# Performance work log

Hardware: AMD Instinct MI355X
Metric: run time of the kernel (lower is better)

## Reference

```python
import jax, jax.numpy as jnp
import numpy as np

B, M, D = 4, 2048, 1024


def setup_inputs() -> dict:
    key = jax.random.key(0)
    k1, k2, k3, k4 = jax.random.split(key, 4)
    x = jax.random.normal(k1, (B, M, D), dtype=jnp.float32)
    scale = 0.02
    wq = jax.random.normal(k2, (D, D), dtype=jnp.float32) * scale
    wk = jax.random.normal(k3, (D, D), dtype=jnp.float32) * scale
    wv = jax.random.normal(k4, (D, D), dtype=jnp.float32) * scale
    return {"x": x, "wq": wq, "wk": wk, "wv": wv}


def _rope_tables(m, d):
    # Faithful to source: phi = 10000 ** (-2*(i-1)/d)  (note the (i-1), incl. i=0)
    i = jnp.arange(d // 2, dtype=jnp.float32)
    phi = jnp.power(10000.0, -2.0 * (i - 1.0) / d)  # [d/2]
    pos = jnp.arange(m, dtype=jnp.float32)
    ang = pos[:, None] * phi[None, :]  # [m, d/2]
    return jnp.cos(ang), jnp.sin(ang)


def _apply_rope(t, cos, sin):
    # Original does t[pos] @ R[pos] (row-vector times rotation matrix):
    #   out_even =  t_even*cos + t_odd*sin
    #   out_odd  = -t_even*sin + t_odd*cos
    te = t[..., 0::2]  # [b, m, d/2]
    to = t[..., 1::2]
    oe = te * cos + to * sin
    oo = -te * sin + to * cos
    return jnp.stack([oe, oo], axis=-1).reshape(t.shape)


def reference(x, wq, wk, wv):
    b, m, d = x.shape
    q = x @ wq.T
    k = x @ wk.T
    v = x @ wv.T
    cos, sin = _rope_tables(m, d)
    qr = _apply_rope(q, cos, sin)
    kr = _apply_rope(k, cos, sin)
    # causal SDPA (dropout disabled for deterministic reference)
    scores = jnp.einsum('bqd,bkd->bqk', qr, kr) / jnp.sqrt(jnp.float32(d))
    causal = jnp.tril(jnp.ones((m, m), dtype=bool))
    scores = jnp.where(causal[None, :, :], scores, jnp.finfo(scores.dtype).min)
    attn = jax.nn.softmax(scores, axis=-1)
    return jnp.einsum('bqk,bkd->bqd', attn, v)
```

## Files before the change

kernel.cpp:

```cpp
#include <hip/hip_runtime.h>
#include <hip/hip_bf16.h>
#include <math.h>


typedef __bf16 bf16x8 __attribute__((ext_vector_type(8)));
typedef float  f32x4  __attribute__((ext_vector_type(4)));

__device__ __forceinline__ ushort f2bf(float f) {
    __hip_bfloat16 h = __float2bfloat16(f);
    return *reinterpret_cast<ushort*>(&h);
}

__device__ __forceinline__ void async_load16(const ushort* g, ushort* l) {
    __builtin_amdgcn_global_load_lds(
        (const __attribute__((address_space(1))) void*)g,
        (__attribute__((address_space(3))) void*)l, 16, 0, 0);
}

__global__ __launch_bounds__(256) void cvt_kernel(
    const float* __restrict__ in, ushort* __restrict__ out, int n4)
{
    int i = blockIdx.x * blockDim.x + threadIdx.x;
    if (i < n4) {
        float4 f = ((const float4*)in)[i];
        ushort4 o;
        o.x = f2bf(f.x); o.y = f2bf(f.y); o.z = f2bf(f.z); o.w = f2bf(f.w);
        ((ushort4*)out)[i] = o;
    }
}

__device__ __forceinline__ void gemm128_core(
    const ushort* __restrict__ A, const ushort* __restrict__ B,
    int lda, int ldb, int m0, int n0, int kIters,
    ushort* As, ushort* Bs, f32x4 acc[4][4])
{
    const int tid  = threadIdx.x;
    const int lane = tid & 63, wave = tid >> 6;
    const int wm = (wave >> 1) * 64, wn = (wave & 1) * 64;
    const int quad = lane >> 4, l16 = lane & 15;
    const int srow = lane >> 2, scol = (lane & 3) * 8;

    const ushort* ag0 = A + (size_t)(m0 + wave * 32 + srow) * lda + scol;
    const ushort* bg0 = B + (size_t)(n0 + wave * 32 + srow) * ldb + scol;
    const ushort* ag1 = ag0 + (size_t)16 * lda;
    const ushort* bg1 = bg0 + (size_t)16 * ldb;
    ushort* la0 = As + (wave * 32) * 32;
    ushort* la1 = As + (wave * 32 + 16) * 32;
    ushort* lb0 = Bs + (wave * 32) * 32;
    ushort* lb1 = Bs + (wave * 32 + 16) * 32;

    for (int kt = 0; kt < kIters; ++kt) {
        const int k0 = kt * 32;
        async_load16(ag0 + k0, la0);
        async_load16(ag1 + k0, la1);
        async_load16(bg0 + k0, lb0);
        async_load16(bg1 + k0, lb1);
        __syncthreads();
        bf16x8 aF[4], bF[4];
#pragma unroll
        for (int i = 0; i < 4; ++i)
            aF[i] = *(const bf16x8*)(As + (wm + i * 16 + l16) * 32 + quad * 8);
#pragma unroll
        for (int j = 0; j < 4; ++j)
            bF[j] = *(const bf16x8*)(Bs + (wn + j * 16 + l16) * 32 + quad * 8);
#pragma unroll
        for (int i = 0; i < 4; ++i)
#pragma unroll
            for (int j = 0; j < 4; ++j)
                acc[i][j] = __builtin_amdgcn_mfma_f32_16x16x32_bf16(aF[i], bF[j], acc[i][j], 0, 0, 0);
        __syncthreads();
    }
}

#define ACC_INIT(acc) \
    _Pragma("unroll") for (int i = 0; i < 4; ++i) \
    _Pragma("unroll") for (int j = 0; j < 4; ++j) \
    _Pragma("unroll") for (int r = 0; r < 4; ++r) acc[i][j][r] = 0.0f;

__global__ __launch_bounds__(256) void qkv_rope_kernel(
    const ushort* __restrict__ xb, const ushort* __restrict__ wq,
    const ushort* __restrict__ wk, const ushort* __restrict__ wv,
    ushort* __restrict__ Qr, ushort* __restrict__ Kr, ushort* __restrict__ VT)
{
    __shared__ __attribute__((aligned(16))) ushort As[128 * 32];
    __shared__ __attribute__((aligned(16))) ushort Bs[128 * 32];
    const int m0 = blockIdx.x * 128;
    const int n0 = blockIdx.y * 128;
    const int z  = blockIdx.z;
    const ushort* W = (z == 0) ? wq : (z == 1) ? wk : wv;

    f32x4 acc[4][4];
    ACC_INIT(acc)
    gemm128_core(xb, W, 1024, 1024, m0, n0, 32, As, Bs, acc);

    const int lane = threadIdx.x & 63, wave = threadIdx.x >> 6;
    const int wm = (wave >> 1) * 64, wn = (wave & 1) * 64;
    const int quad = lane >> 4, l16 = lane & 15;

    if (z < 2) {
        ushort* out = (z == 0) ? Qr : Kr;
#pragma unroll
        for (int j = 0; j < 4; ++j) {
            const int n = n0 + wn + j * 16 + l16;
            const float phi = powf(10000.0f, -2.0f * ((float)(n >> 1) - 1.0f) / 1024.0f);
            float sphi, cphi;
            sincosf(phi, &sphi, &cphi);
#pragma unroll
            for (int i = 0; i < 4; ++i) {
                const int mbase = m0 + wm + i * 16 + quad * 4;
                const int pos0  = mbase & 2047;
                float s, c;
                sincosf((float)pos0 * phi, &s, &c);
#pragma unroll
                for (int r = 0; r < 4; ++r) {
                    float v = acc[i][j][r];
                    float p = __shfl_xor(v, 1);
                    float o = (n & 1) ? (v * c - p * s) : (v * c + p * s);
                    out[(size_t)(mbase + r) * 1024 + n] = f2bf(o);
                    float s2 = s * cphi + c * sphi;
                    c = c * cphi - s * sphi;
                    s = s2;
                }
            }
        }
    } else {
#pragma unroll
        for (int i = 0; i < 4; ++i) {
            const int mbase = m0 + wm + i * 16 + quad * 4;
            const int b = mbase >> 11, pos0 = mbase & 2047;
#pragma unroll
            for (int j = 0; j < 4; ++j) {
                const int n = n0 + wn + j * 16 + l16;
                ushort4 o;
                o.x = f2bf(acc[i][j][0]); o.y = f2bf(acc[i][j][1]);
                o.z = f2bf(acc[i][j][2]); o.w = f2bf(acc[i][j][3]);
                *(ushort4*)(VT + ((size_t)b * 1024 + n) * 2048 + pos0) = o;
            }
        }
    }
}

__global__ __launch_bounds__(256) void scores_kernel(
    const ushort* __restrict__ Qr, const ushort* __restrict__ Kr,
    float* __restrict__ S)
{
    const int m0 = blockIdx.x * 128;
    const int n0 = blockIdx.y * 128;
    if (n0 > m0 + 127) return;
    const int b = blockIdx.z;
    __shared__ __attribute__((aligned(16))) ushort As[128 * 32];
    __shared__ __attribute__((aligned(16))) ushort Bs[128 * 32];
    const ushort* A = Qr + (size_t)b * 2048 * 1024;
    const ushort* B = Kr + (size_t)b * 2048 * 1024;
    float* Sb = S + (size_t)b * 2048 * 2048;

    f32x4 acc[4][4];
    ACC_INIT(acc)
    gemm128_core(A, B, 1024, 1024, m0, n0, 32, As, Bs, acc);

    const int lane = threadIdx.x & 63, wave = threadIdx.x >> 6;
    const int wm = (wave >> 1) * 64, wn = (wave & 1) * 64;
    const int quad = lane >> 4, l16 = lane & 15;
#pragma unroll
    for (int i = 0; i < 4; ++i)
#pragma unroll
        for (int j = 0; j < 4; ++j) {
            const int n = n0 + wn + j * 16 + l16;
#pragma unroll
            for (int r = 0; r < 4; ++r) {
                const int m = m0 + wm + i * 16 + quad * 4 + r;
                Sb[(size_t)m * 2048 + n] = acc[i][j][r] * 0.03125f;
            }
        }
}

__global__ __launch_bounds__(256) void softmax_kernel(
    const float* __restrict__ S, ushort* __restrict__ P)
{
    __shared__ float red[256];
    const int row = blockIdx.x, tid = threadIdx.x, b = blockIdx.y;
    const float* s = S + ((size_t)b * 2048 + row) * 2048;
    ushort*      p = P + ((size_t)b * 2048 + row) * 2048;
    const int nvalid = row + 1;
    const int j0 = tid * 8;

    float v[8];
    float4 f0 = *(const float4*)(s + j0);
    float4 f1 = *(const float4*)(s + j0 + 4);
    v[0]=f0.x; v[1]=f0.y; v[2]=f0.z; v[3]=f0.w;
    v[4]=f1.x; v[5]=f1.y; v[6]=f1.z; v[7]=f1.w;

    float mx = -3.402823466e38f;
#pragma unroll
    for (int u = 0; u < 8; ++u) if (j0 + u < nvalid) mx = fmaxf(mx, v[u]);
    red[tid] = mx; __syncthreads();
    for (int off = 128; off > 0; off >>= 1) {
        if (tid < off) red[tid] = fmaxf(red[tid], red[tid + off]);
        __syncthreads();
    }
    mx = red[0]; __syncthreads();

    float sum = 0.0f;
#pragma unroll
    for (int u = 0; u < 8; ++u) {
        v[u] = (j0 + u < nvalid) ? __expf(v[u] - mx) : 0.0f;
        sum += v[u];
    }
    red[tid] = sum; __syncthreads();
    for (int off = 128; off > 0; off >>= 1) {
        if (tid < off) red[tid] += red[tid + off];
        __syncthreads();
    }
    const float inv = 1.0f / red[0];

    ushort o[8];
#pragma unroll
    for (int u = 0; u < 8; ++u) o[u] = f2bf(v[u] * inv);
    *(int4*)(p + j0) = *(const int4*)o;
}

__global__ __launch_bounds__(256) void pv_kernel(
    const ushort* __restrict__ P, const ushort* __restrict__ VT,
    float* __restrict__ out)
{
    __shared__ __attribute__((aligned(16))) ushort As[128 * 32];
    __shared__ __attribute__((aligned(16))) ushort Bs[128 * 32];
    const int m0 = blockIdx.x * 128;
    const int n0 = blockIdx.y * 128;
    const int b  = blockIdx.z;
    const ushort* A = P + (size_t)b * 2048 * 2048;
    const ushort* B = VT + (size_t)b * 1024 * 2048;
    const int kIters = (m0 + 128) / 32;

    f32x4 acc[4][4];
    ACC_INIT(acc)
    gemm128_core(A, B, 2048, 2048, m0, n0, kIters, As, Bs, acc);

    const int lane = threadIdx.x & 63, wave = threadIdx.x >> 6;
    const int wm = (wave >> 1) * 64, wn = (wave & 1) * 64;
    const int quad = lane >> 4, l16 = lane & 15;
#pragma unroll
    for (int i = 0; i < 4; ++i)
#pragma unroll
        for (int j = 0; j < 4; ++j) {
            const int n = n0 + wn + j * 16 + l16;
#pragma unroll
            for (int r = 0; r < 4; ++r) {
                const int m = m0 + wm + i * 16 + quad * 4 + r;
                out[((size_t)b * 2048 + m) * 1024 + n] = acc[i][j][r];
            }
        }
}

extern "C" void kernel_launch(void* const* d_in, const int* in_sizes, int n_in,
                              void* d_out, int out_size, void* d_ws, size_t ws_size,
                              hipStream_t stream) {
    const float* x  = (const float*)d_in[0];
    const float* wq = (const float*)d_in[1];
    const float* wk = (const float*)d_in[2];
    const float* wv = (const float*)d_in[3];

    const size_t MiB = 1024 * 1024;
    char* ws = (char*)d_ws;
    ushort* xb  = (ushort*)(ws);
    ushort* wqb = (ushort*)(ws +  16 * MiB);
    ushort* wkb = (ushort*)(ws +  18 * MiB);
    ushort* wvb = (ushort*)(ws +  20 * MiB);
    ushort* Qr  = (ushort*)(ws +  22 * MiB);
    ushort* Kr  = (ushort*)(ws +  38 * MiB);
    ushort* VT  = (ushort*)(ws +  54 * MiB);
    float*  S   = (float* )(ws +  70 * MiB);
    ushort* P   = (ushort*)(ws + 134 * MiB);
    float*  out = (float*)d_out;

    cvt_kernel<<<dim3(8192), 256, 0, stream>>>(x,  xb,  2097152);
    cvt_kernel<<<dim3(1024), 256, 0, stream>>>(wq, wqb, 262144);
    cvt_kernel<<<dim3(1024), 256, 0, stream>>>(wk, wkb, 262144);
    cvt_kernel<<<dim3(1024), 256, 0, stream>>>(wv, wvb, 262144);

    qkv_rope_kernel<<<dim3(64, 8, 3),  256, 0, stream>>>(xb, wqb, wkb, wvb, Qr, Kr, VT);
    scores_kernel  <<<dim3(16, 16, 4), 256, 0, stream>>>(Qr, Kr, S);
    softmax_kernel <<<dim3(2048, 4),   256, 0, stream>>>(S, P);
    pv_kernel      <<<dim3(16, 8, 4),  256, 0, stream>>>(P, VT, out);
}
```

Baseline: 305.1 us.

## Fuse QKV projections into one kernel, swizzle LDS, merge conversion launches

```diff
diff --git a/kernel.cpp b/kernel.cpp
--- a/kernel.cpp
+++ b/kernel.cpp
@@ -17,9 +17,16 @@
         (__attribute__((address_space(3))) void*)l, 16, 0, 0);
 }
 
-__global__ __launch_bounds__(256) void cvt_kernel(
-    const float* __restrict__ in, ushort* __restrict__ out, int n4)
-{
+__global__ __launch_bounds__(256) void cvt_all_kernel(
+    const float* __restrict__ x,  const float* __restrict__ wq,
+    const float* __restrict__ wk, const float* __restrict__ wv,
+    ushort* __restrict__ xb, ushort* __restrict__ wqb,
+    ushort* __restrict__ wkb, ushort* __restrict__ wvb)
+{
+    const int t = blockIdx.y;
+    const float* in  = (t == 0) ? x  : (t == 1) ? wq  : (t == 2) ? wk  : wv;
+    ushort*      out = (t == 0) ? xb : (t == 1) ? wqb : (t == 2) ? wkb : wvb;
+    const int n4 = (t == 0) ? 2097152 : 262144;
     int i = blockIdx.x * blockDim.x + threadIdx.x;
     if (i < n4) {
         float4 f = ((const float4*)in)[i];
@@ -38,16 +45,19 @@
     const int lane = tid & 63, wave = tid >> 6;
     const int wm = (wave >> 1) * 64, wn = (wave & 1) * 64;
     const int quad = lane >> 4, l16 = lane & 15;
-    const int srow = lane >> 2, scol = (lane & 3) * 8;
-
-    const ushort* ag0 = A + (size_t)(m0 + wave * 32 + srow) * lda + scol;
-    const ushort* bg0 = B + (size_t)(n0 + wave * 32 + srow) * ldb + scol;
+    const int srow = lane >> 2, c = lane & 3;
+    const int rr   = wave * 32 + srow;
+    const int cc   = c ^ ((rr >> 1) & 3);
+    const int scol = cc * 8;
+
+    const ushort* ag0 = A + (size_t)(m0 + rr) * lda + scol;
+    const ushort* bg0 = B + (size_t)(n0 + rr) * ldb + scol;
     const ushort* ag1 = ag0 + (size_t)16 * lda;
     const ushort* bg1 = bg0 + (size_t)16 * ldb;
     ushort* la0 = As + (wave * 32) * 32;
-    ushort* la1 = As + (wave * 32 + 16) * 32;
+    ushort* la1 = la0 + 16 * 32;
     ushort* lb0 = Bs + (wave * 32) * 32;
-    ushort* lb1 = Bs + (wave * 32 + 16) * 32;
+    ushort* lb1 = lb0 + 16 * 32;
 
     for (int kt = 0; kt < kIters; ++kt) {
         const int k0 = kt * 32;
@@ -58,11 +68,15 @@
         __syncthreads();
         bf16x8 aF[4], bF[4];
 #pragma unroll
-        for (int i = 0; i < 4; ++i)
-            aF[i] = *(const bf16x8*)(As + (wm + i * 16 + l16) * 32 + quad * 8);
-#pragma unroll
-        for (int j = 0; j < 4; ++j)
-            bF[j] = *(const bf16x8*)(Bs + (wn + j * 16 + l16) * 32 + quad * 8);
+        for (int i = 0; i < 4; ++i) {
+            const int r = wm + i * 16 + l16;
+            aF[i] = *(const bf16x8*)(As + r * 32 + ((quad ^ ((r >> 1) & 3)) * 8));
+        }
+#pragma unroll
+        for (int j = 0; j < 4; ++j) {
+            const int r = wn + j * 16 + l16;
+            bF[j] = *(const bf16x8*)(Bs + r * 32 + ((quad ^ ((r >> 1) & 3)) * 8));
+        }
 #pragma unroll
         for (int i = 0; i < 4; ++i)
 #pragma unroll
@@ -72,70 +86,115 @@
     }
 }
 
-#define ACC_INIT(acc) \
+#define ACC_INIT4(acc) \
     _Pragma("unroll") for (int i = 0; i < 4; ++i) \
     _Pragma("unroll") for (int j = 0; j < 4; ++j) \
     _Pragma("unroll") for (int r = 0; r < 4; ++r) acc[i][j][r] = 0.0f;
 
-__global__ __launch_bounds__(256) void qkv_rope_kernel(
+__global__ __launch_bounds__(256, 1) void qkv_fused_kernel(
     const ushort* __restrict__ xb, const ushort* __restrict__ wq,
     const ushort* __restrict__ wk, const ushort* __restrict__ wv,
     ushort* __restrict__ Qr, ushort* __restrict__ Kr, ushort* __restrict__ VT)
 {
     __shared__ __attribute__((aligned(16))) ushort As[128 * 32];
-    __shared__ __attribute__((aligned(16))) ushort Bs[128 * 32];
+    __shared__ __attribute__((aligned(16))) ushort Bs[3][128 * 32];
     const int m0 = blockIdx.x * 128;
     const int n0 = blockIdx.y * 128;
-    const int z  = blockIdx.z;
-    const ushort* W = (z == 0) ? wq : (z == 1) ? wk : wv;
-
-    f32x4 acc[4][4];
-    ACC_INIT(acc)
-    gemm128_core(xb, W, 1024, 1024, m0, n0, 32, As, Bs, acc);
-
-    const int lane = threadIdx.x & 63, wave = threadIdx.x >> 6;
+
+    const int tid  = threadIdx.x;
+    const int lane = tid & 63, wave = tid >> 6;
     const int wm = (wave >> 1) * 64, wn = (wave & 1) * 64;
     const int quad = lane >> 4, l16 = lane & 15;
-
-    if (z < 2) {
-        ushort* out = (z == 0) ? Qr : Kr;
+    const int srow = lane >> 2, c = lane & 3;
+    const int rr   = wave * 32 + srow;
+    const int cc   = c ^ ((rr >> 1) & 3);
+    const int scol = cc * 8;
+
+    const ushort* ag0 = xb + (size_t)(m0 + rr) * 1024 + scol;
+    const ushort* ag1 = ag0 + 16 * 1024;
+    const ushort* wg[3];
+    wg[0] = wq + (size_t)(n0 + rr) * 1024 + scol;
+    wg[1] = wk + (size_t)(n0 + rr) * 1024 + scol;
+    wg[2] = wv + (size_t)(n0 + rr) * 1024 + scol;
+    ushort* la0 = As + (wave * 32) * 32;
+    ushort* la1 = la0 + 16 * 32;
+
+    f32x4 acc[3][4][4];
+#pragma unroll
+    for (int z = 0; z < 3; ++z) ACC_INIT4(acc[z])
+
+    for (int kt = 0; kt < 32; ++kt) {
+        const int k0 = kt * 32;
+        async_load16(ag0 + k0, la0);
+        async_load16(ag1 + k0, la1);
+#pragma unroll
+        for (int z = 0; z < 3; ++z) {
+            ushort* lb = Bs[z] + (wave * 32) * 32;
+            async_load16(wg[z] + k0, lb);
+            async_load16(wg[z] + 16 * 1024 + k0, lb + 16 * 32);
+        }
+        __syncthreads();
+        bf16x8 aF[4];
+#pragma unroll
+        for (int i = 0; i < 4; ++i) {
+            const int r = wm + i * 16 + l16;
+            aF[i] = *(const bf16x8*)(As + r * 32 + ((quad ^ ((r >> 1) & 3)) * 8));
+        }
+#pragma unroll
+        for (int z = 0; z < 3; ++z) {
+            bf16x8 bF[4];
+#pragma unroll
+            for (int j = 0; j < 4; ++j) {
+                const int r = wn + j * 16 + l16;
+                bF[j] = *(const bf16x8*)(Bs[z] + r * 32 + ((quad ^ ((r >> 1) & 3)) * 8));
+            }
+#pragma unroll
+            for (int i = 0; i < 4; ++i)
+#pragma unroll
+                for (int j = 0; j < 4; ++j)
+                    acc[z][i][j] = __builtin_amdgcn_mfma_f32_16x16x32_bf16(aF[i], bF[j], acc[z][i][j], 0, 0, 0);
+        }
+        __syncthreads();
+    }
+
+#pragma unroll
+    for (int j = 0; j < 4; ++j) {
+        const int n = n0 + wn + j * 16 + l16;
+        const float phi = powf(10000.0f, -2.0f * ((float)(n >> 1) - 1.0f) / 1024.0f);
+        float sphi, cphi;
+        sincosf(phi, &sphi, &cphi);
+#pragma unroll
+        for (int i = 0; i < 4; ++i) {
+            const int mbase = m0 + wm + i * 16 + quad * 4;
+            const int pos0  = mbase & 2047;
+            float s, cz;
+            sincosf((float)pos0 * phi, &s, &cz);
+#pragma unroll
+            for (int r = 0; r < 4; ++r) {
+                const size_t row = (size_t)(mbase + r);
+                float vq = acc[0][i][j][r];
+                float pq = __shfl_xor(vq, 1);
+                Qr[row * 1024 + n] = f2bf((n & 1) ? (vq * cz - pq * s) : (vq * cz + pq * s));
+                float vk = acc[1][i][j][r];
+                float pk = __shfl_xor(vk, 1);
+                Kr[row * 1024 + n] = f2bf((n & 1) ? (vk * cz - pk * s) : (vk * cz + pk * s));
+                float s2 = s * cphi + cz * sphi;
+                cz = cz * cphi - s * sphi;
+                s  = s2;
+            }
+        }
+    }
+#pragma unroll
+    for (int i = 0; i < 4; ++i) {
+        const int mbase = m0 + wm + i * 16 + quad * 4;
+        const int b = mbase >> 11, pos0 = mbase & 2047;
 #pragma unroll
         for (int j = 0; j < 4; ++j) {
             const int n = n0 + wn + j * 16 + l16;
-            const float phi = powf(10000.0f, -2.0f * ((float)(n >> 1) - 1.0f) / 1024.0f);
-            float sphi, cphi;
-            sincosf(phi, &sphi, &cphi);
-#pragma unroll
-            for (int i = 0; i < 4; ++i) {
-                const int mbase = m0 + wm + i * 16 + quad * 4;
-                const int pos0  = mbase & 2047;
-                float s, c;
-                sincosf((float)pos0 * phi, &s, &c);
-#pragma unroll
-                for (int r = 0; r < 4; ++r) {
-                    float v = acc[i][j][r];
-                    float p = __shfl_xor(v, 1);
-                    float o = (n & 1) ? (v * c - p * s) : (v * c + p * s);
-                    out[(size_t)(mbase + r) * 1024 + n] = f2bf(o);
-                    float s2 = s * cphi + c * sphi;
-                    c = c * cphi - s * sphi;
-                    s = s2;
-                }
-            }
-        }
-    } else {
-#pragma unroll
-        for (int i = 0; i < 4; ++i) {
-            const int mbase = m0 + wm + i * 16 + quad * 4;
-            const int b = mbase >> 11, pos0 = mbase & 2047;
-#pragma unroll
-            for (int j = 0; j < 4; ++j) {
-                const int n = n0 + wn + j * 16 + l16;
-                ushort4 o;
-                o.x = f2bf(acc[i][j][0]); o.y = f2bf(acc[i][j][1]);
-                o.z = f2bf(acc[i][j][2]); o.w = f2bf(acc[i][j][3]);
-                *(ushort4*)(VT + ((size_t)b * 1024 + n) * 2048 + pos0) = o;
-            }
+            ushort4 o;
+            o.x = f2bf(acc[2][i][j][0]); o.y = f2bf(acc[2][i][j][1]);
+            o.z = f2bf(acc[2][i][j][2]); o.w = f2bf(acc[2][i][j][3]);
+            *(ushort4*)(VT + ((size_t)b * 1024 + n) * 2048 + pos0) = o;
         }
     }
 }
@@ -155,7 +214,7 @@
     float* Sb = S + (size_t)b * 2048 * 2048;
 
     f32x4 acc[4][4];
-    ACC_INIT(acc)
+    ACC_INIT4(acc)
     gemm128_core(A, B, 1024, 1024, m0, n0, 32, As, Bs, acc);
 
     const int lane = threadIdx.x & 63, wave = threadIdx.x >> 6;
@@ -233,7 +292,7 @@
     const int kIters = (m0 + 128) / 32;
 
     f32x4 acc[4][4];
-    ACC_INIT(acc)
+    ACC_INIT4(acc)
     gemm128_core(A, B, 2048, 2048, m0, n0, kIters, As, Bs, acc);
 
     const int lane = threadIdx.x & 63, wave = threadIdx.x >> 6;
@@ -273,12 +332,8 @@
     ushort* P   = (ushort*)(ws + 134 * MiB);
     float*  out = (float*)d_out;
 
-    cvt_kernel<<<dim3(8192), 256, 0, stream>>>(x,  xb,  2097152);
-    cvt_kernel<<<dim3(1024), 256, 0, stream>>>(wq, wqb, 262144);
-    cvt_kernel<<<dim3(1024), 256, 0, stream>>>(wk, wkb, 262144);
-    cvt_kernel<<<dim3(1024), 256, 0, stream>>>(wv, wvb, 262144);
-
-    qkv_rope_kernel<<<dim3(64, 8, 3),  256, 0, stream>>>(xb, wqb, wkb, wvb, Qr, Kr, VT);
+    cvt_all_kernel <<<dim3(8192, 4),   256, 0, stream>>>(x, wq, wk, wv, xb, wqb, wkb, wvb);
+    qkv_fused_kernel<<<dim3(64, 8),    256, 0, stream>>>(xb, wqb, wkb, wvb, Qr, Kr, VT);
     scores_kernel  <<<dim3(16, 16, 4), 256, 0, stream>>>(Qr, Kr, S);
     softmax_kernel <<<dim3(2048, 4),   256, 0, stream>>>(S, P);
     pv_kernel      <<<dim3(16, 8, 4),  256, 0, stream>>>(P, VT, out);
```

Measured after the change: 319.9 us. 1.05x slower.
